# Kernel tuning notes

Hardware: AMD Instinct MI355X
Metric: run time of the kernel (lower is better)

Reference implementation:

```python
import jax, jax.numpy as jnp
import numpy as np

B, N, DIM, H, DH = 4, 4096, 1024, 16, 64
INNER = H * DH


def setup_inputs() -> dict:
    key = jax.random.key(0)
    k1, k2, k3, k4 = jax.random.split(key, 4)
    x = jax.random.normal(k1, (B, N, DIM), dtype=jnp.float32)
    mask = jax.random.randint(k2, (B, N), 0, 2).astype(bool)
    Wqkv = jax.random.normal(k3, (DIM, 3 * INNER), dtype=jnp.float32) * (DIM ** -0.5)
    Wout = jax.random.normal(k4, (INNER, DIM), dtype=jnp.float32) * (INNER ** -0.5)
    bout = jnp.zeros((DIM,), dtype=jnp.float32)
    return {"x": x, "mask": mask, "Wqkv": Wqkv, "Wout": Wout, "bout": bout}


def _split_heads(t):
    b, n, _ = t.shape
    return t.reshape(b, n, H, DH).transpose(0, 2, 1, 3)  # b h n d


def reference(x, mask, Wqkv, Wout, bout):
    qkv = x @ Wqkv                      # [b, n, 3*inner]
    q, k, v = jnp.split(qkv, 3, axis=-1)
    q, k, v = map(_split_heads, (q, k, v))  # [b, h, n, d]
    q = jax.nn.elu(q) + 1.0
    k = jax.nn.elu(k) + 1.0
    m = mask[:, None, :, None]          # [b, 1, n, 1]
    k = jnp.where(m, k, 0.0)
    v = jnp.where(m, v, 0.0)
    kv = jnp.einsum('bhnd,bhne->bhde', k, v)      # [b, h, d, d]
    out = jnp.einsum('bhnd,bhde->bhne', q, kv)    # [b, h, n, d]
    z = 1.0 / (jnp.einsum('bhnd,bhd->bhn', q, k.sum(axis=2)) + 1e-6)
    out = out * z[..., None]
    out = out.transpose(0, 2, 1, 3).reshape(x.shape[0], -1, INNER)  # [b, n, inner]
    return out @ Wout + bout
```

## Files before the change

### kernel.cpp

```cpp
#include <hip/hip_runtime.h>
#include <hip/hip_bf16.h>
#include <cstddef>
#include <cstdint>

#define B_     4
#define N_     4096
#define DIM_   1024
#define H_     16
#define DH_    64
#define INNER_ 1024
#define MTOK   (B_ * N_)
#define QKVC   (3 * INNER_)
#define NCH    16
#define CHUNK  (N_ / NCH)

typedef __attribute__((ext_vector_type(8))) short short8;
typedef __attribute__((ext_vector_type(4))) float f32x4;

__device__ __forceinline__ float elu1(float x) {
    return x > 0.f ? x + 1.f : __expf(x);
}
__device__ __forceinline__ unsigned short f2bf(float f) {
    __hip_bfloat16 h = __float2bfloat16(f);
    return __builtin_bit_cast(unsigned short, h);
}
__device__ __forceinline__ float bf2f(unsigned short u) {
    __hip_bfloat16 h = __builtin_bit_cast(__hip_bfloat16, u);
    return __bfloat162float(h);
}

__device__ __forceinline__ void gload16(const void* g, void* l) {
    __builtin_amdgcn_global_load_lds(
        (const __attribute__((address_space(1))) unsigned int*)g,
        (__attribute__((address_space(3))) unsigned int*)l, 16, 0, 0);
}

__global__ __launch_bounds__(256) void cast_bf16(
    const float* __restrict__ src, unsigned short* __restrict__ dst, long n8)
{
    const long stride = (long)gridDim.x * 256;
    for (long i = (long)blockIdx.x * 256 + threadIdx.x; i < n8; i += stride) {
        const float4 f0 = reinterpret_cast<const float4*>(src)[2 * i];
        const float4 f1 = reinterpret_cast<const float4*>(src)[2 * i + 1];
        short8 u;
        u[0] = (short)f2bf(f0.x); u[1] = (short)f2bf(f0.y);
        u[2] = (short)f2bf(f0.z); u[3] = (short)f2bf(f0.w);
        u[4] = (short)f2bf(f1.x); u[5] = (short)f2bf(f1.y);
        u[6] = (short)f2bf(f1.z); u[7] = (short)f2bf(f1.w);
        reinterpret_cast<short8*>(dst)[i] = u;
    }
}

__global__ __launch_bounds__(256) void transpose_cast(
    const float* __restrict__ src, unsigned short* __restrict__ dst,
    int R, int C)
{
    __shared__ float t[32][33];
    const int r0 = blockIdx.x * 32, c0 = blockIdx.y * 32;
    const int tx = threadIdx.x & 31, ty = threadIdx.x >> 5;
#pragma unroll
    for (int i = 0; i < 4; ++i)
        t[ty * 4 + i][tx] = src[(size_t)(r0 + ty * 4 + i) * C + c0 + tx];
    __syncthreads();
#pragma unroll
    for (int i = 0; i < 4; ++i)
        dst[(size_t)(c0 + ty * 4 + i) * R + r0 + tx] = f2bf(t[tx][ty * 4 + i]);
}

template<int OUT_BF16, int HAS_BIAS>
__global__ __launch_bounds__(512, 2) void gemm256(
    const unsigned short* __restrict__ A,
    const unsigned short* __restrict__ BT,
    void* __restrict__ Cv,
    const float* __restrict__ bias,
    int M, int N, int K, int lda, int ldb, int ldc)
{
    __shared__ __align__(16) unsigned short lA[2][256 * 64];
    __shared__ __align__(16) unsigned short lB[2][256 * 64];

    const int tid = threadIdx.x;
    const int wv  = tid >> 6;
    const int ln  = tid & 63;
    const int wr  = wv >> 2;
    const int wc  = wv & 3;

    const int nwg = gridDim.x;
    int wg = blockIdx.x;
    {
        const int q = nwg >> 3, r = nwg & 7;
        const int xcd = wg & 7, lid = wg >> 3;
        wg = (xcd < r ? xcd * (q + 1) : r * (q + 1) + (xcd - r) * q) + lid;
    }
    const int ncol = N >> 8;
    const int bx = wg % ncol;
    const int by = wg / ncol;
    const int row0 = by << 8;
    const int col0 = bx << 8;

    const int l8    = ln >> 3;
    const int sslot = ((ln & 7) ^ l8) << 3;

    const int lr16 = ln & 15;
    const int kc   = ln >> 4;
    const int sw   = lr16 & 7;
    const int soff0 = (kc ^ sw) << 3;
    const int soff1 = ((4 + kc) ^ sw) << 3;

    f32x4 acc[8][4];
#pragma unroll
    for (int m = 0; m < 8; ++m)
#pragma unroll
        for (int n = 0; n < 4; ++n) acc[m][n] = f32x4{0.f, 0.f, 0.f, 0.f};

    const int NT = K >> 6;

#pragma unroll
    for (int i = 0; i < 4; ++i) {
        const int lr = wv * 32 + i * 8;
        gload16(&A [(size_t)(row0 + lr + l8) * lda + sslot], &lA[0][lr * 64]);
        gload16(&BT[(size_t)(col0 + lr + l8) * ldb + sslot], &lB[0][lr * 64]);
    }
    __syncthreads();

    for (int t = 0; t < NT; ++t) {
        const int cur = t & 1;
        const unsigned short* bufA = lA[cur];
        const unsigned short* bufB = lB[cur];
        short8 bf[4][2];
#pragma unroll
        for (int p = 0; p < 4; ++p) {
            short8 af[2][2];
#pragma unroll
            for (int mi = 0; mi < 2; ++mi) {
                const int row = wr * 128 + (p * 2 + mi) * 16 + lr16;
                af[mi][0] = *reinterpret_cast<const short8*>(&bufA[row * 64 + soff0]);
                af[mi][1] = *reinterpret_cast<const short8*>(&bufA[row * 64 + soff1]);
            }
            if (p == 0) {
#pragma unroll
                for (int n = 0; n < 4; ++n) {
                    const int row = wc * 64 + n * 16 + lr16;
                    bf[n][0] = *reinterpret_cast<const short8*>(&bufB[row * 64 + soff0]);
                    bf[n][1] = *reinterpret_cast<const short8*>(&bufB[row * 64 + soff1]);
                }
                if (t + 1 < NT) {
                    const int k0 = (t + 1) << 6;
                    unsigned short* nA = lA[cur ^ 1];
                    unsigned short* nB = lB[cur ^ 1];
#pragma unroll
                    for (int i = 0; i < 4; ++i) {
                        const int lr = wv * 32 + i * 8;
                        gload16(&A [(size_t)(row0 + lr + l8) * lda + k0 + sslot],
                                &nA[lr * 64]);
                        gload16(&BT[(size_t)(col0 + lr + l8) * ldb + k0 + sslot],
                                &nB[lr * 64]);
                    }
                }
            }
            __builtin_amdgcn_s_barrier();
            __builtin_amdgcn_sched_barrier(0);
            __builtin_amdgcn_s_setprio(1);
#pragma unroll
            for (int mi = 0; mi < 2; ++mi)
#pragma unroll
                for (int n = 0; n < 4; ++n) {
                    acc[p * 2 + mi][n] = __builtin_amdgcn_mfma_f32_16x16x32_bf16(
                        af[mi][0], bf[n][0], acc[p * 2 + mi][n], 0, 0, 0);
                    acc[p * 2 + mi][n] = __builtin_amdgcn_mfma_f32_16x16x32_bf16(
                        af[mi][1], bf[n][1], acc[p * 2 + mi][n], 0, 0, 0);
                }
            __builtin_amdgcn_s_setprio(0);
            __builtin_amdgcn_sched_barrier(0);
            if (p < 3) {
                __builtin_amdgcn_s_barrier();
                __builtin_amdgcn_sched_barrier(0);
            }
        }
        __syncthreads();
    }

    const int orow = (ln >> 4) << 2;
    const int ocol = ln & 15;
#pragma unroll
    for (int m = 0; m < 8; ++m) {
#pragma unroll
        for (int n = 0; n < 4; ++n) {
            const int c = col0 + wc * 64 + n * 16 + ocol;
            float bv = 0.f;
            if constexpr (HAS_BIAS) bv = bias[c];
#pragma unroll
            for (int r2 = 0; r2 < 4; ++r2) {
                const int rr = row0 + wr * 128 + m * 16 + orow + r2;
                const float o = acc[m][n][r2] + bv;
                if constexpr (OUT_BF16)
                    ((unsigned short*)Cv)[(size_t)rr * ldc + c] = f2bf(o);
                else
                    ((float*)Cv)[(size_t)rr * ldc + c] = o;
            }
        }
    }
}

__global__ __launch_bounds__(256) void kv_partial(
    const unsigned short* __restrict__ kvbf, const int* __restrict__ mask,
    float* __restrict__ part)
{
    const int bh = blockIdx.x;
    const int ch = blockIdx.y;
    const int b = bh / H_;
    const int h = bh % H_;
    const int n0 = ch * CHUNK;

    __shared__ float kl[8][68];
    __shared__ float vl[8][68];

    const int tid = threadIdx.x;
    const int tx = tid & 15;
    const int ty = tid >> 4;

    const int lw = tid >> 7;
    const int lr2 = (tid >> 4) & 7;
    const int lc = (tid & 15) << 2;

    float acc[4][4] = {};
    float ks = 0.f;

    for (int s = 0; s < CHUNK; s += 8) {
        const int n = n0 + s + lr2;
        ushort4 u4 = *reinterpret_cast<const ushort4*>(
            &kvbf[(size_t)(b * N_ + n) * 2048 + (lw << 10) + h * 64 + lc]);
        const int m = mask[b * N_ + n];
        float f[4] = { bf2f(u4.x), bf2f(u4.y), bf2f(u4.z), bf2f(u4.w) };
        if (!m) { f[0] = f[1] = f[2] = f[3] = 0.f; }
        else if (lw == 0) {
#pragma unroll
            for (int i = 0; i < 4; ++i) f[i] = elu1(f[i]);
        }
        __syncthreads();
        float* dst = lw ? &vl[lr2][lc] : &kl[lr2][lc];
        dst[0] = f[0]; dst[1] = f[1]; dst[2] = f[2]; dst[3] = f[3];
        __syncthreads();
#pragma unroll
        for (int r = 0; r < 8; ++r) {
            float kd[4], vv[4];
#pragma unroll
            for (int i = 0; i < 4; ++i) kd[i] = kl[r][(ty << 2) + i];
#pragma unroll
            for (int j = 0; j < 4; ++j) vv[j] = vl[r][(tx << 2) + j];
#pragma unroll
            for (int i = 0; i < 4; ++i)
#pragma unroll
                for (int j = 0; j < 4; ++j) acc[i][j] += kd[i] * vv[j];
        }
        if (tid < 64) {
#pragma unroll
            for (int r = 0; r < 8; ++r) ks += kl[r][tid];
        }
    }

    float* p = part + ((size_t)bh * NCH + ch) * 4160;
#pragma unroll
    for (int i = 0; i < 4; ++i)
#pragma unroll
        for (int j = 0; j < 4; ++j)
            p[((ty << 2) + i) * 64 + (tx << 2) + j] = acc[i][j];
    if (tid < 64) p[4096 + tid] = ks;
}

__global__ __launch_bounds__(256) void kv_reduce(
    const float* __restrict__ part, float* __restrict__ kvf)
{
    const int bh = blockIdx.x;
    for (int idx = threadIdx.x; idx < 4160; idx += 256) {
        float s = 0.f;
        for (int c = 0; c < NCH; ++c)
            s += part[((size_t)bh * NCH + c) * 4160 + idx];
        kvf[(size_t)bh * 4160 + idx] = s;
    }
}

__global__ __launch_bounds__(256) void attn_apply(
    const unsigned short* __restrict__ qbf, const float* __restrict__ kvf,
    unsigned short* __restrict__ attnbf)
{
    const int bh = blockIdx.x;
    const int nt = blockIdx.y;
    const int b = bh / H_;
    const int h = bh % H_;
    const int n0 = nt * 64;

    __shared__ float kv[64][65];
    __shared__ float fq[64][65];
    __shared__ float ks[64];

    const int tid = threadIdx.x;

#pragma unroll
    for (int i = 0; i < 16; ++i) {
        const int idx = i * 256 + tid;
        kv[idx >> 6][idx & 63] = kvf[(size_t)bh * 4160 + idx];
    }
    if (tid < 64) ks[tid] = kvf[(size_t)bh * 4160 + 4096 + tid];
#pragma unroll
    for (int i = 0; i < 16; ++i) {
        const int idx = i * 256 + tid;
        const int tok = idx >> 6;
        const int c = idx & 63;
        const float val =
            bf2f(qbf[(size_t)(b * N_ + n0 + tok) * INNER_ + h * 64 + c]);
        fq[tok][c] = elu1(val);
    }
    __syncthreads();

    const int tx = tid & 15;
    const int ty = tid >> 4;
    float acc[4][4] = {};
    float den[4] = {};

    for (int d = 0; d < 64; ++d) {
        float qv[4], kvv[4];
#pragma unroll
        for (int i = 0; i < 4; ++i) qv[i] = fq[(ty << 2) + i][d];
#pragma unroll
        for (int j = 0; j < 4; ++j) kvv[j] = kv[d][(tx << 2) + j];
        const float ksd = ks[d];
#pragma unroll
        for (int i = 0; i < 4; ++i) {
            den[i] += qv[i] * ksd;
#pragma unroll
            for (int j = 0; j < 4; ++j) acc[i][j] += qv[i] * kvv[j];
        }
    }

#pragma unroll
    for (int i = 0; i < 4; ++i) {
        const float z = 1.f / (den[i] + 1e-6f);
        const int n = n0 + (ty << 2) + i;
#pragma unroll
        for (int j = 0; j < 4; ++j)
            attnbf[(size_t)(b * N_ + n) * INNER_ + h * 64 + (tx << 2) + j] =
                f2bf(acc[i][j] * z);
    }
}

extern "C" void kernel_launch(void* const* d_in, const int* in_sizes, int n_in,
                              void* d_out, int out_size, void* d_ws, size_t ws_size,
                              hipStream_t stream)
{
    const float* x    = (const float*)d_in[0];
    const int*   mask = (const int*)d_in[1];
    const float* Wqkv = (const float*)d_in[2];
    const float* Wout = (const float*)d_in[3];
    const float* bout = (const float*)d_in[4];
    float* out = (float*)d_out;

    const size_t need = 127156224;
    if (ws_size < need) return;

    char* base = (char*)d_ws;
    unsigned short* xbf    = (unsigned short*)base;
    unsigned short* attnbf = xbf;
    unsigned short* kvbf   = (unsigned short*)(base + 33554432);
    unsigned short* wqkvT  = (unsigned short*)(base + 100663296);
    unsigned short* woutT  = (unsigned short*)(base + 106954752);
    float* part = (float*)(base + 109051904);
    float* kvf  = (float*)(base + 126091264);
    unsigned short* qbf = (unsigned short*)d_out;

    cast_bf16<<<dim3(2048), dim3(256), 0, stream>>>(
        x, xbf, (long)MTOK * DIM_ / 8);
    transpose_cast<<<dim3(32, 96), dim3(256), 0, stream>>>(Wqkv, wqkvT, DIM_, QKVC);
    transpose_cast<<<dim3(32, 32), dim3(256), 0, stream>>>(Wout, woutT, INNER_, INNER_);

    gemm256<1, 0><<<dim3(64 * 4), dim3(512), 0, stream>>>(
        xbf, wqkvT, qbf, nullptr, MTOK, 1024, DIM_, DIM_, DIM_, 1024);
    gemm256<1, 0><<<dim3(64 * 8), dim3(512), 0, stream>>>(
        xbf, wqkvT + (size_t)1024 * 1024, kvbf, nullptr,
        MTOK, 2048, DIM_, DIM_, DIM_, 2048);

    kv_partial<<<dim3(B_ * H_, NCH), dim3(256), 0, stream>>>(kvbf, mask, part);
    kv_reduce<<<dim3(B_ * H_), dim3(256), 0, stream>>>(part, kvf);

    attn_apply<<<dim3(B_ * H_, N_ / 64), dim3(256), 0, stream>>>(qbf, kvf, attnbf);

    gemm256<0, 1><<<dim3(64 * 4), dim3(512), 0, stream>>>(
        attnbf, woutT, out, bout, MTOK, INNER_, INNER_, INNER_, INNER_, INNER_);
}
```

Before: 287.1 us.

## Fuse ELU and mask into QKV GEMM epilogue and move KV/attn to MFMA

The Q GEMM epilogue now applies ELU+1, and the KV GEMM epilogue applies ELU and the mask and writes K/V transposed (feature-major). kv_partial and the attention-apply kernel are rewritten to use bf16 MFMA instead of scalar FMA loops. KV is split into hi/lo bf16 parts to limit precision loss. This removes the scalar outer-product cost and the separate elementwise passes, at the cost of bf16 rounding of K, V and KV, and of transposed stores with a strided pattern.

```diff
diff --git a/kernel.cpp b/kernel.cpp
--- a/kernel.cpp
+++ b/kernel.cpp
@@ -67,12 +67,13 @@
         dst[(size_t)(c0 + ty * 4 + i) * R + r0 + tx] = f2bf(t[tx][ty * 4 + i]);
 }
 
-template<int OUT_BF16, int HAS_BIAS>
+template<int EPI, int HAS_BIAS>
 __global__ __launch_bounds__(512, 2) void gemm256(
     const unsigned short* __restrict__ A,
     const unsigned short* __restrict__ BT,
     void* __restrict__ Cv,
     const float* __restrict__ bias,
+    const int* __restrict__ msk,
     int M, int N, int K, int lda, int ldb, int ldc)
 {
     __shared__ __align__(16) unsigned short lA[2][256 * 64];
@@ -183,163 +184,249 @@
     const int ocol = ln & 15;
 #pragma unroll
     for (int m = 0; m < 8; ++m) {
+        const int rrb = row0 + wr * 128 + m * 16 + orow;
+        int mv[4];
+        if constexpr (EPI == 2) {
+            const int4 m4 = *reinterpret_cast<const int4*>(&msk[rrb]);
+            mv[0] = m4.x; mv[1] = m4.y; mv[2] = m4.z; mv[3] = m4.w;
+        }
 #pragma unroll
         for (int n = 0; n < 4; ++n) {
             const int c = col0 + wc * 64 + n * 16 + ocol;
-            float bv = 0.f;
-            if constexpr (HAS_BIAS) bv = bias[c];
-#pragma unroll
-            for (int r2 = 0; r2 < 4; ++r2) {
-                const int rr = row0 + wr * 128 + m * 16 + orow + r2;
-                const float o = acc[m][n][r2] + bv;
-                if constexpr (OUT_BF16)
-                    ((unsigned short*)Cv)[(size_t)rr * ldc + c] = f2bf(o);
-                else
-                    ((float*)Cv)[(size_t)rr * ldc + c] = o;
+            if constexpr (EPI == 2) {
+                const bool isk = (c < 1024);
+                ushort4 st;
+#pragma unroll
+                for (int r2 = 0; r2 < 4; ++r2) {
+                    float o = acc[m][n][r2];
+                    o = mv[r2] ? (isk ? elu1(o) : o) : 0.f;
+                    ((unsigned short*)&st)[r2] = f2bf(o);
+                }
+                *reinterpret_cast<ushort4*>(
+                    &((unsigned short*)Cv)[(size_t)c * ldc + rrb]) = st;
+            } else {
+                float bv = 0.f;
+                if constexpr (HAS_BIAS) bv = bias[c];
+#pragma unroll
+                for (int r2 = 0; r2 < 4; ++r2) {
+                    const int rr = rrb + r2;
+                    float o = acc[m][n][r2] + bv;
+                    if constexpr (EPI == 1) {
+                        o = elu1(o);
+                        ((unsigned short*)Cv)[(size_t)rr * ldc + c] = f2bf(o);
+                    } else {
+                        ((float*)Cv)[(size_t)rr * ldc + c] = o;
+                    }
+                }
             }
         }
     }
 }
 
 __global__ __launch_bounds__(256) void kv_partial(
-    const unsigned short* __restrict__ kvbf, const int* __restrict__ mask,
-    float* __restrict__ part)
+    const unsigned short* __restrict__ kvT, float* __restrict__ part)
 {
     const int bh = blockIdx.x;
     const int ch = blockIdx.y;
-    const int b = bh / H_;
-    const int h = bh % H_;
-    const int n0 = ch * CHUNK;
-
-    __shared__ float kl[8][68];
-    __shared__ float vl[8][68];
+    const int b = bh / H_, h = bh % H_;
+    const int tok0 = b * N_ + ch * CHUNK;
+
+    __shared__ __align__(16) unsigned short kt[64 * 64];
+    __shared__ __align__(16) unsigned short vt[64 * 64];
+    __shared__ float ksr[4][64];
 
     const int tid = threadIdx.x;
-    const int tx = tid & 15;
-    const int ty = tid >> 4;
-
-    const int lw = tid >> 7;
-    const int lr2 = (tid >> 4) & 7;
-    const int lc = (tid & 15) << 2;
-
-    float acc[4][4] = {};
-    float ks = 0.f;
-
-    for (int s = 0; s < CHUNK; s += 8) {
-        const int n = n0 + s + lr2;
-        ushort4 u4 = *reinterpret_cast<const ushort4*>(
-            &kvbf[(size_t)(b * N_ + n) * 2048 + (lw << 10) + h * 64 + lc]);
-        const int m = mask[b * N_ + n];
-        float f[4] = { bf2f(u4.x), bf2f(u4.y), bf2f(u4.z), bf2f(u4.w) };
-        if (!m) { f[0] = f[1] = f[2] = f[3] = 0.f; }
-        else if (lw == 0) {
-#pragma unroll
-            for (int i = 0; i < 4; ++i) f[i] = elu1(f[i]);
-        }
+    const int wv = tid >> 6, ln = tid & 63;
+    const int wr = wv >> 1, wc = wv & 1;
+    const int l8 = ln >> 3;
+    const int sslot = ((ln & 7) ^ l8) << 3;
+    const int lr16 = ln & 15;
+    const int kc = ln >> 4;
+    const int sw = lr16 & 7;
+
+    const size_t krow = (size_t)(h * 64) * MTOK;
+    const size_t vrow = (size_t)(1024 + h * 64) * MTOK;
+
+    f32x4 acc[2][2];
+#pragma unroll
+    for (int i = 0; i < 2; ++i)
+#pragma unroll
+        for (int j = 0; j < 2; ++j) acc[i][j] = f32x4{0.f, 0.f, 0.f, 0.f};
+
+    const int kd = tid & 63, kq = tid >> 6;
+    float ksacc = 0.f;
+
+    for (int st = 0; st < 4; ++st) {
+        const int tb = tok0 + st * 64;
         __syncthreads();
-        float* dst = lw ? &vl[lr2][lc] : &kl[lr2][lc];
-        dst[0] = f[0]; dst[1] = f[1]; dst[2] = f[2]; dst[3] = f[3];
+#pragma unroll
+        for (int i = 0; i < 2; ++i) {
+            const int rb = (wv * 2 + i) * 8;
+            gload16(&kvT[krow + (size_t)(rb + l8) * MTOK + tb + sslot], &kt[rb * 64]);
+            gload16(&kvT[vrow + (size_t)(rb + l8) * MTOK + tb + sslot], &vt[rb * 64]);
+        }
         __syncthreads();
 #pragma unroll
-        for (int r = 0; r < 8; ++r) {
-            float kd[4], vv[4];
-#pragma unroll
-            for (int i = 0; i < 4; ++i) kd[i] = kl[r][(ty << 2) + i];
-#pragma unroll
-            for (int j = 0; j < 4; ++j) vv[j] = vl[r][(tx << 2) + j];
-#pragma unroll
-            for (int i = 0; i < 4; ++i)
-#pragma unroll
-                for (int j = 0; j < 4; ++j) acc[i][j] += kd[i] * vv[j];
-        }
-        if (tid < 64) {
-#pragma unroll
-            for (int r = 0; r < 8; ++r) ks += kl[r][tid];
-        }
-    }
+        for (int ks = 0; ks < 2; ++ks) {
+            const int soff = ((ks * 4 + kc) ^ sw) << 3;
+            short8 af[2], bf[2];
+#pragma unroll
+            for (int mi = 0; mi < 2; ++mi)
+                af[mi] = *reinterpret_cast<const short8*>(
+                    &kt[(wr * 32 + mi * 16 + lr16) * 64 + soff]);
+#pragma unroll
+            for (int ni = 0; ni < 2; ++ni)
+                bf[ni] = *reinterpret_cast<const short8*>(
+                    &vt[(wc * 32 + ni * 16 + lr16) * 64 + soff]);
+#pragma unroll
+            for (int mi = 0; mi < 2; ++mi)
+#pragma unroll
+                for (int ni = 0; ni < 2; ++ni)
+                    acc[mi][ni] = __builtin_amdgcn_mfma_f32_16x16x32_bf16(
+                        af[mi], bf[ni], acc[mi][ni], 0, 0, 0);
+        }
+#pragma unroll
+        for (int sl = 0; sl < 2; ++sl) {
+            const int phys = (kq * 2 + sl) ^ (kd & 7);
+            short8 v = *reinterpret_cast<const short8*>(&kt[kd * 64 + phys * 8]);
+#pragma unroll
+            for (int e = 0; e < 8; ++e) ksacc += bf2f((unsigned short)v[e]);
+        }
+    }
+    ksr[kq][kd] = ksacc;
+    __syncthreads();
 
     float* p = part + ((size_t)bh * NCH + ch) * 4160;
-#pragma unroll
-    for (int i = 0; i < 4; ++i)
-#pragma unroll
-        for (int j = 0; j < 4; ++j)
-            p[((ty << 2) + i) * 64 + (tx << 2) + j] = acc[i][j];
-    if (tid < 64) p[4096 + tid] = ks;
+    const int orow = (ln >> 4) << 2;
+    const int ocol = ln & 15;
+#pragma unroll
+    for (int mi = 0; mi < 2; ++mi)
+#pragma unroll
+        for (int ni = 0; ni < 2; ++ni) {
+            const int d0 = wr * 32 + mi * 16 + orow;
+            const int e  = wc * 32 + ni * 16 + ocol;
+#pragma unroll
+            for (int r = 0; r < 4; ++r)
+                p[(d0 + r) * 64 + e] = acc[mi][ni][r];
+        }
+    if (tid < 64)
+        p[4096 + tid] = ksr[0][tid] + ksr[1][tid] + ksr[2][tid] + ksr[3][tid];
 }
 
 __global__ __launch_bounds__(256) void kv_reduce(
-    const float* __restrict__ part, float* __restrict__ kvf)
+    const float* __restrict__ part, unsigned short* __restrict__ kvtb,
+    float* __restrict__ ksumf)
 {
     const int bh = blockIdx.x;
-    for (int idx = threadIdx.x; idx < 4160; idx += 256) {
+    for (int idx = threadIdx.x; idx < 4096; idx += 256) {
         float s = 0.f;
         for (int c = 0; c < NCH; ++c)
             s += part[((size_t)bh * NCH + c) * 4160 + idx];
-        kvf[(size_t)bh * 4160 + idx] = s;
-    }
-}
-
-__global__ __launch_bounds__(256) void attn_apply(
-    const unsigned short* __restrict__ qbf, const float* __restrict__ kvf,
+        const int d = idx >> 6, e = idx & 63;
+        const unsigned short hi = f2bf(s);
+        const float lo = s - bf2f(hi);
+        kvtb[(size_t)bh * 8192 + e * 64 + d] = hi;
+        kvtb[(size_t)bh * 8192 + 4096 + e * 64 + d] = f2bf(lo);
+    }
+    if (threadIdx.x < 64) {
+        float s = 0.f;
+        for (int c = 0; c < NCH; ++c)
+            s += part[((size_t)bh * NCH + c) * 4160 + 4096 + threadIdx.x];
+        ksumf[bh * 64 + threadIdx.x] = s;
+    }
+}
+
+__global__ __launch_bounds__(256) void attn_mfma(
+    const unsigned short* __restrict__ qbf,
+    const unsigned short* __restrict__ kvtb,
+    const float* __restrict__ ksumf,
     unsigned short* __restrict__ attnbf)
 {
-    const int bh = blockIdx.x;
-    const int nt = blockIdx.y;
-    const int b = bh / H_;
-    const int h = bh % H_;
-    const int n0 = nt * 64;
-
-    __shared__ float kv[64][65];
-    __shared__ float fq[64][65];
-    __shared__ float ks[64];
+    const int bh = blockIdx.x, tt = blockIdx.y;
+    const int b = bh / H_, h = bh % H_;
+    const int tok0 = b * N_ + tt * 256;
+
+    __shared__ __align__(16) unsigned short qt[256 * 64];
+    __shared__ float den[256];
 
     const int tid = threadIdx.x;
-
-#pragma unroll
-    for (int i = 0; i < 16; ++i) {
-        const int idx = i * 256 + tid;
-        kv[idx >> 6][idx & 63] = kvf[(size_t)bh * 4160 + idx];
-    }
-    if (tid < 64) ks[tid] = kvf[(size_t)bh * 4160 + 4096 + tid];
-#pragma unroll
-    for (int i = 0; i < 16; ++i) {
-        const int idx = i * 256 + tid;
-        const int tok = idx >> 6;
-        const int c = idx & 63;
-        const float val =
-            bf2f(qbf[(size_t)(b * N_ + n0 + tok) * INNER_ + h * 64 + c]);
-        fq[tok][c] = elu1(val);
+    const int wv = tid >> 6, ln = tid & 63;
+    const int l8 = ln >> 3;
+    const int sslot = ((ln & 7) ^ l8) << 3;
+    const int lr16 = ln & 15;
+    const int kc = ln >> 4;
+
+    const unsigned short* kvb = kvtb + (size_t)bh * 8192;
+    short8 bhf[4][2], blf[4][2];
+#pragma unroll
+    for (int n = 0; n < 4; ++n)
+#pragma unroll
+        for (int ks = 0; ks < 2; ++ks) {
+            const int off = (n * 16 + lr16) * 64 + ks * 32 + kc * 8;
+            bhf[n][ks] = *reinterpret_cast<const short8*>(&kvb[off]);
+            blf[n][ks] = *reinterpret_cast<const short8*>(&kvb[4096 + off]);
+        }
+
+#pragma unroll
+    for (int i = 0; i < 8; ++i) {
+        const int rb = wv * 64 + i * 8;
+        gload16(&qbf[(size_t)(tok0 + rb + l8) * INNER_ + h * 64 + sslot],
+                &qt[rb * 64]);
+    }
+
+    {
+        float dsum = 0.f;
+        const unsigned short* qr = &qbf[(size_t)(tok0 + tid) * INNER_ + h * 64];
+        const float* ksp = &ksumf[bh * 64];
+#pragma unroll
+        for (int j = 0; j < 8; ++j) {
+            short8 v = *reinterpret_cast<const short8*>(&qr[j * 8]);
+#pragma unroll
+            for (int e = 0; e < 8; ++e)
+                dsum += bf2f((unsigned short)v[e]) * ksp[j * 8 + e];
+        }
+        den[tid] = dsum;
     }
     __syncthreads();
 
-    const int tx = tid & 15;
-    const int ty = tid >> 4;
-    float acc[4][4] = {};
-    float den[4] = {};
-
-    for (int d = 0; d < 64; ++d) {
-        float qv[4], kvv[4];
-#pragma unroll
-        for (int i = 0; i < 4; ++i) qv[i] = fq[(ty << 2) + i][d];
-#pragma unroll
-        for (int j = 0; j < 4; ++j) kvv[j] = kv[d][(tx << 2) + j];
-        const float ksd = ks[d];
-#pragma unroll
-        for (int i = 0; i < 4; ++i) {
-            den[i] += qv[i] * ksd;
-#pragma unroll
-            for (int j = 0; j < 4; ++j) acc[i][j] += qv[i] * kvv[j];
-        }
-    }
-
-#pragma unroll
-    for (int i = 0; i < 4; ++i) {
-        const float z = 1.f / (den[i] + 1e-6f);
-        const int n = n0 + (ty << 2) + i;
-#pragma unroll
-        for (int j = 0; j < 4; ++j)
-            attnbf[(size_t)(b * N_ + n) * INNER_ + h * 64 + (tx << 2) + j] =
-                f2bf(acc[i][j] * z);
+    f32x4 acc[4][4];
+#pragma unroll
+    for (int m = 0; m < 4; ++m)
+#pragma unroll
+        for (int n = 0; n < 4; ++n) acc[m][n] = f32x4{0.f, 0.f, 0.f, 0.f};
+
+#pragma unroll
+    for (int ks = 0; ks < 2; ++ks) {
+        const int soff = ((ks * 4 + kc) ^ (lr16 & 7)) << 3;
+        short8 af[4];
+#pragma unroll
+        for (int m = 0; m < 4; ++m)
+            af[m] = *reinterpret_cast<const short8*>(
+                &qt[(wv * 64 + m * 16 + lr16) * 64 + soff]);
+#pragma unroll
+        for (int m = 0; m < 4; ++m)
+#pragma unroll
+            for (int n = 0; n < 4; ++n) {
+                acc[m][n] = __builtin_amdgcn_mfma_f32_16x16x32_bf16(
+                    af[m], bhf[n][ks], acc[m][n], 0, 0, 0);
+                acc[m][n] = __builtin_amdgcn_mfma_f32_16x16x32_bf16(
+                    af[m], blf[n][ks], acc[m][n], 0, 0, 0);
+            }
+    }
+
+    const int orow = (ln >> 4) << 2;
+    const int ocol = ln & 15;
+#pragma unroll
+    for (int m = 0; m < 4; ++m) {
+        const int rl = wv * 64 + m * 16 + orow;
+#pragma unroll
+        for (int r = 0; r < 4; ++r) {
+            const float z = 1.f / (den[rl + r] + 1e-6f);
+            const size_t orow_g = (size_t)(tok0 + rl + r) * INNER_ + h * 64;
+#pragma unroll
+            for (int n = 0; n < 4; ++n)
+                attnbf[orow_g + n * 16 + ocol] = f2bf(acc[m][n][r] * z);
+        }
     }
 }
 
@@ -360,11 +447,12 @@
     char* base = (char*)d_ws;
     unsigned short* xbf    = (unsigned short*)base;
     unsigned short* attnbf = xbf;
-    unsigned short* kvbf   = (unsigned short*)(base + 33554432);
+    unsigned short* kvT    = (unsigned short*)(base + 33554432);
     unsigned short* wqkvT  = (unsigned short*)(base + 100663296);
     unsigned short* woutT  = (unsigned short*)(base + 106954752);
-    float* part = (float*)(base + 109051904);
-    float* kvf  = (float*)(base + 126091264);
+    float* part  = (float*)(base + 109051904);
+    unsigned short* kvtb = (unsigned short*)(base + 126091264);
+    float* ksumf = (float*)(base + 127139840);
     unsigned short* qbf = (unsigned short*)d_out;
 
     cast_bf16<<<dim3(2048), dim3(256), 0, stream>>>(
@@ -373,16 +461,17 @@
     transpose_cast<<<dim3(32, 32), dim3(256), 0, stream>>>(Wout, woutT, INNER_, INNER_);
 
     gemm256<1, 0><<<dim3(64 * 4), dim3(512), 0, stream>>>(
-        xbf, wqkvT, qbf, nullptr, MTOK, 1024, DIM_, DIM_, DIM_, 1024);
-    gemm256<1, 0><<<dim3(64 * 8), dim3(512), 0, stream>>>(
-        xbf, wqkvT + (size_t)1024 * 1024, kvbf, nullptr,
-        MTOK, 2048, DIM_, DIM_, DIM_, 2048);
-
-    kv_partial<<<dim3(B_ * H_, NCH), dim3(256), 0, stream>>>(kvbf, mask, part);
-    kv_reduce<<<dim3(B_ * H_), dim3(256), 0, stream>>>(part, kvf);
-
-    attn_apply<<<dim3(B_ * H_, N_ / 64), dim3(256), 0, stream>>>(qbf, kvf, attnbf);
+        xbf, wqkvT, qbf, nullptr, nullptr, MTOK, 1024, DIM_, DIM_, DIM_, 1024);
+    gemm256<2, 0><<<dim3(64 * 8), dim3(512), 0, stream>>>(
+        xbf, wqkvT + (size_t)1024 * 1024, kvT, nullptr, mask,
+        MTOK, 2048, DIM_, DIM_, DIM_, MTOK);
+
+    kv_partial<<<dim3(B_ * H_, NCH), dim3(256), 0, stream>>>(kvT, part);
+    kv_reduce<<<dim3(B_ * H_), dim3(256), 0, stream>>>(part, kvtb, ksumf);
+
+    attn_mfma<<<dim3(B_ * H_, N_ / 256), dim3(256), 0, stream>>>(
+        qbf, kvtb, ksumf, attnbf);
 
     gemm256<0, 1><<<dim3(64 * 4), dim3(512), 0, stream>>>(
-        attnbf, woutT, out, bout, MTOK, INNER_, INNER_, INNER_, INNER_, INNER_);
-}
+        attnbf, woutT, out, bout, nullptr, MTOK, INNER_, INNER_, INNER_, INNER_, INNER_);
+}
```

New measurement: 268.8 us. 6.4% less time.
